# Kernel optimization log

Hardware: AMD Instinct MI355X
Metric: run time of the kernel (lower is better)

## Reference

```python
import jax, jax.numpy as jnp
import numpy as np

NUM_HEADS = 16

def setup_inputs() -> dict:
    key = jax.random.key(0)
    k1, k2, k3 = jax.random.split(key, 3)
    B, N, C = 4, 4096, 1024
    x = jax.random.normal(k1, (B, N, C), dtype=jnp.float32)
    y = jax.random.normal(k2, (B, N, C), dtype=jnp.float32)
    # nn.Linear(embed_dim, embed_dim): weight [C, C], bias [C]
    W_proj = jax.random.normal(k3, (C, C), dtype=jnp.float32) * (1.0 / np.sqrt(C))
    b_proj = jnp.zeros((C,), dtype=jnp.float32)
    return {"x": x, "y": y, "W_proj": W_proj, "b_proj": b_proj}

def reference(x, y, W_proj, b_proj):
    B, N, C = x.shape
    H = NUM_HEADS
    d = C // H
    # NOTE: no head transpose in the original -> scores are over the HEAD axis.
    q = x.reshape(B, N, H, d)
    k = y.reshape(B, N, H, d)
    v = y.reshape(B, N, H, d)
    # attn: [B, N, H, H], per-token head-to-head scores
    attn = jnp.einsum('bnhd,bngd->bnhg', q, k) / jnp.sqrt(jnp.asarray(d, x.dtype))
    attn = jax.nn.softmax(attn, axis=-1)
    # dropout(p=0.1) is identity in eval mode
    o = jnp.einsum('bnhg,bngd->bnhd', attn, v)          # [B, N, H, d]
    # x.transpose(1, 2).reshape(B, N, C) in torch:
    o = jnp.transpose(o, (0, 2, 1, 3)).reshape(B, N, C)
    out = o @ W_proj.T + b_proj
    return out
```

## Files before the change

### kernel.cpp

```cpp
#include <hip/hip_runtime.h>
#include <hip/hip_bf16.h>
#include <stdint.h>

typedef __attribute__((ext_vector_type(8))) short bf16x8;
typedef __attribute__((ext_vector_type(4))) short bf16x4;
typedef __attribute__((ext_vector_type(4))) float f32x4;
typedef __attribute__((ext_vector_type(4))) int   i32x4;

static __device__ __forceinline__ short f2bs(float f) {
  __hip_bfloat16 h = __float2bfloat16(f);
  return __builtin_bit_cast(short, h);
}

__device__ __forceinline__ void gload_lds16(const void* g, void* l) {
  auto* gp = reinterpret_cast<__attribute__((address_space(1))) uint32_t*>((uintptr_t)g);
  auto* lp = reinterpret_cast<__attribute__((address_space(3))) uint32_t*>((uintptr_t)l);
  __builtin_amdgcn_global_load_lds(gp, lp, 16, 0, 0);
}

__global__ __launch_bounds__(256) void attn_kernel(
    const float* __restrict__ x, const float* __restrict__ y,
    __hip_bfloat16* __restrict__ A)
{
  const int wid  = threadIdx.x >> 6;
  const int lane = threadIdx.x & 63;
  const int tok  = blockIdx.x * 4 + wid;
  const int b    = tok >> 12;
  const int n    = tok & 4095;

  const float* xr = x + (size_t)tok * 1024;
  const float* yr = y + (size_t)tok * 1024;

  const int c  = lane & 15;
  const int qq = lane >> 4;

  const int fbase = c * 64 + qq * 8;
  bf16x8 yf[2], xf[2];
  #pragma unroll
  for (int kk = 0; kk < 2; ++kk) {
    const float4 a0 = *(const float4*)(yr + fbase + kk * 32);
    const float4 a1 = *(const float4*)(yr + fbase + kk * 32 + 4);
    const float4 b0 = *(const float4*)(xr + fbase + kk * 32);
    const float4 b1 = *(const float4*)(xr + fbase + kk * 32 + 4);
    yf[kk] = bf16x8{f2bs(a0.x), f2bs(a0.y), f2bs(a0.z), f2bs(a0.w),
                    f2bs(a1.x), f2bs(a1.y), f2bs(a1.z), f2bs(a1.w)};
    xf[kk] = bf16x8{f2bs(b0.x), f2bs(b0.y), f2bs(b0.z), f2bs(b0.w),
                    f2bs(b1.x), f2bs(b1.y), f2bs(b1.z), f2bs(b1.w)};
  }

  f32x4 acc = {0.f, 0.f, 0.f, 0.f};
  acc = __builtin_amdgcn_mfma_f32_16x16x32_bf16(yf[0], xf[0], acc, 0, 0, 0);
  acc = __builtin_amdgcn_mfma_f32_16x16x32_bf16(yf[1], xf[1], acc, 0, 0, 0);

  float sc[4];
  #pragma unroll
  for (int r = 0; r < 4; ++r) sc[r] = acc[r] * 0.125f;
  float mx = fmaxf(fmaxf(sc[0], sc[1]), fmaxf(sc[2], sc[3]));
  mx = fmaxf(mx, __shfl_xor(mx, 16));
  mx = fmaxf(mx, __shfl_xor(mx, 32));
  float e[4];
  #pragma unroll
  for (int r = 0; r < 4; ++r) e[r] = __expf(sc[r] - mx);
  float sm = (e[0] + e[1]) + (e[2] + e[3]);
  sm += __shfl_xor(sm, 16);
  sm += __shfl_xor(sm, 32);
  const float inv = 1.0f / sm;
  float p[4];
  #pragma unroll
  for (int r = 0; r < 4; ++r) p[r] = e[r] * inv;

  f32x4 o[4];
  #pragma unroll
  for (int q = 0; q < 4; ++q) o[q] = f32x4{0.f, 0.f, 0.f, 0.f};

#if __has_builtin(__builtin_amdgcn_mfma_f32_16x16x16bf16_1k)
  const bf16x4 pa = {f2bs(p[0]), f2bs(p[1]), f2bs(p[2]), f2bs(p[3])};
  #pragma unroll
  for (int q = 0; q < 4; ++q) {
    bf16x4 bq;
    #pragma unroll
    for (int j = 0; j < 4; ++j)
      bq[j] = f2bs(yr[(qq * 4 + j) * 64 + q * 16 + c]);
    o[q] = __builtin_amdgcn_mfma_f32_16x16x16bf16_1k(pa, bq, o[q], 0, 0, 0);
  }
#else
  const int u0 = ((int)(unsigned short)f2bs(p[1]) << 16) | (unsigned short)f2bs(p[0]);
  const int u1 = ((int)(unsigned short)f2bs(p[3]) << 16) | (unsigned short)f2bs(p[2]);
  const int s0 = c + 32 * qq;
  int a0 = __shfl(u0, s0), a1 = __shfl(u1, s0);
  int a2 = __shfl(u0, s0 + 16), a3 = __shfl(u1, s0 + 16);
  const bool valid = (qq < 2);
  if (!valid) { a0 = 0; a1 = 0; a2 = 0; a3 = 0; }
  const bf16x8 a8 = __builtin_bit_cast(bf16x8, i32x4{a0, a1, a2, a3});
  #pragma unroll
  for (int q = 0; q < 4; ++q) {
    bf16x8 b8;
    #pragma unroll
    for (int j = 0; j < 8; ++j) {
      const int g = (qq * 8 + j) & 15;
      const float v = yr[g * 64 + q * 16 + c];
      b8[j] = valid ? f2bs(v) : (short)0;
    }
    o[q] = __builtin_amdgcn_mfma_f32_16x16x32_bf16(a8, b8, o[q], 0, 0, 0);
  }
#endif

  const size_t base = ((size_t)b * 4096 + (n >> 4)) * 1024 + ((n & 15) << 6) + c;
  #pragma unroll
  for (int q = 0; q < 4; ++q)
    #pragma unroll
    for (int r = 0; r < 4; ++r) {
      const int h = qq * 4 + r;
      A[base + (size_t)h * 262144 + q * 16] = __float2bfloat16(o[q][r]);
    }
}

__global__ __launch_bounds__(256) void wcvt_kernel(const float* __restrict__ w,
                                                   __hip_bfloat16* __restrict__ wb)
{
  const int i = (blockIdx.x * 256 + threadIdx.x) * 4;
  const float4 v = *(const float4*)(w + i);
  wb[i + 0] = __float2bfloat16(v.x);
  wb[i + 1] = __float2bfloat16(v.y);
  wb[i + 2] = __float2bfloat16(v.z);
  wb[i + 3] = __float2bfloat16(v.w);
}

#define NT 16

#define FENCE asm volatile("" ::: "memory")
#define BAR   __builtin_amdgcn_s_barrier()

#define STAGE_A(toff, b) do {                                           \
    gload_lds16(aSrc + (toff),          aDst + (b) * 32768);            \
    gload_lds16(aSrc + (toff) + 131072, aDst + (b) * 32768 + 8192);     \
    gload_lds16(aSrc + (toff) + 262144, aDst + (b) * 32768 + 16384);    \
    gload_lds16(aSrc + (toff) + 393216, aDst + (b) * 32768 + 24576);    \
  } while (0)

#define STAGE_B(toff, b) do {                                           \
    gload_lds16(bSrc + (toff),          bDst + (b) * 32768);            \
    gload_lds16(bSrc + (toff) + 131072, bDst + (b) * 32768 + 8192);     \
    gload_lds16(bSrc + (toff) + 262144, bDst + (b) * 32768 + 16384);    \
    gload_lds16(bSrc + (toff) + 393216, bDst + (b) * 32768 + 24576);    \
  } while (0)

__global__ __launch_bounds__(512, 2) void gemm256(
    const __hip_bfloat16* __restrict__ A,
    const __hip_bfloat16* __restrict__ Bw,
    const float* __restrict__ bias,
    float* __restrict__ C)
{
  constexpr int K = 1024, Nn = 1024;
  __shared__ char ldsA[2 * 32768];
  __shared__ char ldsB[2 * 32768];

  const int tid  = threadIdx.x;
  const int lane = tid & 63;
  const int wid  = tid >> 6;
  const int wr   = wid >> 2;
  const int wc   = wid & 3;

  const int bid = blockIdx.x;
  const int nb  = (bid & 7) * 32 + (bid >> 3);
  const int mBase = (nb >> 2) * 256;
  const int nBase = (nb & 3) * 256;

  const int srow = tid >> 3;
  const int pcb  = (tid & 7) << 4;
  const int lcb  = pcb ^ ((srow & 7) << 4);
  const char* aSrc = (const char*)A  + ((size_t)(mBase + srow) * K) * 2 + lcb;
  const char* bSrc = (const char*)Bw + ((size_t)(nBase + srow) * K) * 2 + lcb;
  char* aDst = ldsA + tid * 16;
  char* bDst = ldsB + tid * 16;

  const int fr = lane & 15;
  const int kq = lane >> 4;
  const int xr = (fr & 7) << 4;
  const int ofk0 = ((kq << 4))      ^ xr;
  const int ofk1 = (64 + (kq << 4)) ^ xr;
  const char* aRow = ldsA + (wr * 128 + fr) * 128;
  const char* bRow = ldsB + (wc * 64  + fr) * 128;

  f32x4 acc[8][4];
  #pragma unroll
  for (int m = 0; m < 8; ++m)
    #pragma unroll
    for (int n = 0; n < 4; ++n) acc[m][n] = f32x4{0.f, 0.f, 0.f, 0.f};

  STAGE_A(0, 0);
  STAGE_B(0, 0);
  asm volatile("s_waitcnt vmcnt(0)" ::: "memory");
  BAR;

  for (int t = 0; t < NT; ++t) {
    const int cur  = t & 1;
    const int nxt  = cur ^ 1;
    const int toff = (t + 1) * 128;
    const char* aR = aRow + cur * 32768;
    const char* bR = bRow + cur * 32768;
    bf16x8 Af[4], Bf[4];

    if (t + 1 < NT) STAGE_A(toff, nxt);
    #pragma unroll
    for (int n = 0; n < 4; ++n) Bf[n] = *(const bf16x8*)(bR + n * 2048 + ofk0);
    #pragma unroll
    for (int m = 0; m < 4; ++m) Af[m] = *(const bf16x8*)(aR + m * 2048 + ofk0);
    FENCE; BAR;
    asm volatile("s_waitcnt lgkmcnt(0)" ::: "memory");
    __builtin_amdgcn_sched_barrier(0);
    __builtin_amdgcn_s_setprio(1);
    #pragma unroll
    for (int m = 0; m < 4; ++m)
      #pragma unroll
      for (int n = 0; n < 4; ++n)
        acc[m][n] = __builtin_amdgcn_mfma_f32_16x16x32_bf16(Af[m], Bf[n], acc[m][n], 0, 0, 0);
    __builtin_amdgcn_s_setprio(0);
    FENCE; BAR;

    if (t + 1 < NT) STAGE_B(toff, nxt);
    #pragma unroll
    for (int m = 0; m < 4; ++m) Af[m] = *(const bf16x8*)(aR + (4 + m) * 2048 + ofk0);
    FENCE; BAR;
    asm volatile("s_waitcnt lgkmcnt(0)" ::: "memory");
    __builtin_amdgcn_sched_barrier(0);
    __builtin_amdgcn_s_setprio(1);
    #pragma unroll
    for (int m = 0; m < 4; ++m)
      #pragma unroll
      for (int n = 0; n < 4; ++n)
        acc[4 + m][n] = __builtin_amdgcn_mfma_f32_16x16x32_bf16(Af[m], Bf[n], acc[4 + m][n], 0, 0, 0);
    __builtin_amdgcn_s_setprio(0);
    FENCE; BAR;

    #pragma unroll
    for (int n = 0; n < 4; ++n) Bf[n] = *(const bf16x8*)(bR + n * 2048 + ofk1);
    #pragma unroll
    for (int m = 0; m < 4; ++m) Af[m] = *(const bf16x8*)(aR + m * 2048 + ofk1);
    FENCE; BAR;
    asm volatile("s_waitcnt lgkmcnt(0)" ::: "memory");
    __builtin_amdgcn_sched_barrier(0);
    __builtin_amdgcn_s_setprio(1);
    #pragma unroll
    for (int m = 0; m < 4; ++m)
      #pragma unroll
      for (int n = 0; n < 4; ++n)
        acc[m][n] = __builtin_amdgcn_mfma_f32_16x16x32_bf16(Af[m], Bf[n], acc[m][n], 0, 0, 0);
    __builtin_amdgcn_s_setprio(0);
    FENCE; BAR;

    #pragma unroll
    for (int m = 0; m < 4; ++m) Af[m] = *(const bf16x8*)(aR + (4 + m) * 2048 + ofk1);
    FENCE; BAR;
    asm volatile("s_waitcnt lgkmcnt(0)" ::: "memory");
    __builtin_amdgcn_sched_barrier(0);
    __builtin_amdgcn_s_setprio(1);
    #pragma unroll
    for (int m = 0; m < 4; ++m)
      #pragma unroll
      for (int n = 0; n < 4; ++n)
        acc[4 + m][n] = __builtin_amdgcn_mfma_f32_16x16x32_bf16(Af[m], Bf[n], acc[4 + m][n], 0, 0, 0);
    __builtin_amdgcn_s_setprio(0);
    if (t + 1 < NT) asm volatile("s_waitcnt vmcnt(0)" ::: "memory");
    FENCE; BAR;
  }

  const int fq = lane >> 4;
  #pragma unroll
  for (int n = 0; n < 4; ++n) {
    const int col = nBase + wc * 64 + n * 16 + fr;
    const float bv = bias[col];
    #pragma unroll
    for (int m = 0; m < 8; ++m) {
      const int row0 = mBase + wr * 128 + m * 16 + fq * 4;
      #pragma unroll
      for (int r = 0; r < 4; ++r)
        C[(size_t)(row0 + r) * Nn + col] = acc[m][n][r] + bv;
    }
  }
}

extern "C" void kernel_launch(void* const* d_in, const int* in_sizes, int n_in,
                              void* d_out, int out_size, void* d_ws, size_t ws_size,
                              hipStream_t stream) {
  const float* x    = (const float*)d_in[0];
  const float* y    = (const float*)d_in[1];
  const float* W    = (const float*)d_in[2];
  const float* bias = (const float*)d_in[3];
  float* out = (float*)d_out;

  __hip_bfloat16* Abuf = (__hip_bfloat16*)d_ws;
  __hip_bfloat16* Wbuf = (__hip_bfloat16*)((char*)d_ws + (size_t)16384 * 1024 * 2);

  wcvt_kernel<<<1024, 256, 0, stream>>>(W, Wbuf);
  attn_kernel<<<4096, 256, 0, stream>>>(x, y, Abuf);
  gemm256<<<256, 512, 0, stream>>>(Abuf, Wbuf, bias, out);
}
```

Before: 76.39 us.

## Split GEMM tile prefetch into finer chunks with partial vmcnt waits and peeled epilogue

Global-to-LDS staging of the next A/B K-tile is split into pairs of loads spread across the four MFMA phases. Full vmcnt(0) drains are replaced with vmcnt(2) partial waits so only the chunks needed next must arrive. The last iteration is peeled so the stores for the first half of the accumulators overlap the final MFMA phase. This aims to hide load latency and epilogue store cost, at the risk of tighter ordering assumptions around the partial waits and LDS buffer reuse.

```diff
diff --git a/kernel.cpp b/kernel.cpp
--- a/kernel.cpp
+++ b/kernel.cpp
@@ -130,20 +130,30 @@
 
 #define FENCE asm volatile("" ::: "memory")
 #define BAR   __builtin_amdgcn_s_barrier()
-
-#define STAGE_A(toff, b) do {                                           \
-    gload_lds16(aSrc + (toff),          aDst + (b) * 32768);            \
-    gload_lds16(aSrc + (toff) + 131072, aDst + (b) * 32768 + 8192);     \
-    gload_lds16(aSrc + (toff) + 262144, aDst + (b) * 32768 + 16384);    \
-    gload_lds16(aSrc + (toff) + 393216, aDst + (b) * 32768 + 24576);    \
-  } while (0)
-
-#define STAGE_B(toff, b) do {                                           \
-    gload_lds16(bSrc + (toff),          bDst + (b) * 32768);            \
-    gload_lds16(bSrc + (toff) + 131072, bDst + (b) * 32768 + 8192);     \
-    gload_lds16(bSrc + (toff) + 262144, bDst + (b) * 32768 + 16384);    \
-    gload_lds16(bSrc + (toff) + 393216, bDst + (b) * 32768 + 24576);    \
-  } while (0)
+#define LGKM0 asm volatile("s_waitcnt lgkmcnt(0)" ::: "memory")
+#define VM2   asm volatile("s_waitcnt vmcnt(2)" ::: "memory")
+#define VM0   asm volatile("s_waitcnt vmcnt(0)" ::: "memory")
+#define SB0   __builtin_amdgcn_sched_barrier(0)
+#define SP1   __builtin_amdgcn_s_setprio(1)
+#define SP0   __builtin_amdgcn_s_setprio(0)
+
+#define SGA(j, toff, bufn) gload_lds16(aSrc + (toff) + (j) * 131072, aDst + (bufn) * 32768 + (j) * 8192)
+#define SGB(j, toff, bufn) gload_lds16(bSrc + (toff) + (j) * 131072, bDst + (bufn) * 32768 + (j) * 8192)
+
+#define MFMA16(MO)                                                         \
+  _Pragma("unroll")                                                        \
+  for (int m = 0; m < 4; ++m)                                              \
+    _Pragma("unroll")                                                      \
+    for (int n = 0; n < 4; ++n)                                            \
+      acc[(MO) + m][n] = __builtin_amdgcn_mfma_f32_16x16x32_bf16(Af[m], Bf[n], acc[(MO) + m][n], 0, 0, 0)
+
+#define READ_B(OF)                                                         \
+  _Pragma("unroll")                                                        \
+  for (int n = 0; n < 4; ++n) Bf[n] = *(const bf16x8*)(bR + n * 2048 + (OF))
+
+#define READ_A(MO, OF)                                                     \
+  _Pragma("unroll")                                                        \
+  for (int m = 0; m < 4; ++m) Af[m] = *(const bf16x8*)(aR + ((MO) + m) * 2048 + (OF))
 
 __global__ __launch_bounds__(512, 2) void gemm256(
     const __hip_bfloat16* __restrict__ A,
@@ -167,8 +177,7 @@
   const int nBase = (nb & 3) * 256;
 
   const int srow = tid >> 3;
-  const int pcb  = (tid & 7) << 4;
-  const int lcb  = pcb ^ ((srow & 7) << 4);
+  const int lcb  = ((tid & 7) << 4) ^ ((srow & 7) << 4);
   const char* aSrc = (const char*)A  + ((size_t)(mBase + srow) * K) * 2 + lcb;
   const char* bSrc = (const char*)Bw + ((size_t)(nBase + srow) * K) * 2 + lcb;
   char* aDst = ldsA + tid * 16;
@@ -188,12 +197,12 @@
     #pragma unroll
     for (int n = 0; n < 4; ++n) acc[m][n] = f32x4{0.f, 0.f, 0.f, 0.f};
 
-  STAGE_A(0, 0);
-  STAGE_B(0, 0);
-  asm volatile("s_waitcnt vmcnt(0)" ::: "memory");
+  SGB(0, 0, 0); SGB(1, 0, 0); SGB(2, 0, 0); SGB(3, 0, 0);
+  SGA(0, 0, 0); SGA(2, 0, 0); SGA(1, 0, 0); SGA(3, 0, 0);
+  VM2;
   BAR;
 
-  for (int t = 0; t < NT; ++t) {
+  for (int t = 0; t < NT - 1; ++t) {
     const int cur  = t & 1;
     const int nxt  = cur ^ 1;
     const int toff = (t + 1) * 128;
@@ -201,77 +210,72 @@
     const char* bR = bRow + cur * 32768;
     bf16x8 Af[4], Bf[4];
 
-    if (t + 1 < NT) STAGE_A(toff, nxt);
-    #pragma unroll
-    for (int n = 0; n < 4; ++n) Bf[n] = *(const bf16x8*)(bR + n * 2048 + ofk0);
-    #pragma unroll
-    for (int m = 0; m < 4; ++m) Af[m] = *(const bf16x8*)(aR + m * 2048 + ofk0);
+    SGB(0, toff, nxt); SGB(1, toff, nxt);
+    READ_B(ofk0); READ_A(0, ofk0);
+    FENCE; BAR; LGKM0; SB0;
+    SP1; MFMA16(0); SP0;
+    VM2; FENCE; BAR;
+
+    SGB(2, toff, nxt); SGB(3, toff, nxt);
+    READ_A(4, ofk0);
+    FENCE; BAR; LGKM0; SB0;
+    SP1; MFMA16(4); SP0;
     FENCE; BAR;
-    asm volatile("s_waitcnt lgkmcnt(0)" ::: "memory");
-    __builtin_amdgcn_sched_barrier(0);
-    __builtin_amdgcn_s_setprio(1);
-    #pragma unroll
-    for (int m = 0; m < 4; ++m)
+
+    SGA(0, toff, nxt); SGA(2, toff, nxt);
+    READ_B(ofk1); READ_A(0, ofk1);
+    FENCE; BAR; LGKM0; SB0;
+    SP1; MFMA16(0); SP0;
+    FENCE; BAR;
+
+    SGA(1, toff, nxt); SGA(3, toff, nxt);
+    READ_A(4, ofk1);
+    FENCE; BAR; LGKM0; SB0;
+    SP1; MFMA16(4); SP0;
+    VM2; FENCE; BAR;
+  }
+
+  const int fq = lane >> 4;
+  {
+    const char* aR = aRow + ((NT - 1) & 1) * 32768;
+    const char* bR = bRow + ((NT - 1) & 1) * 32768;
+    bf16x8 Af[4], Bf[4];
+
+    READ_B(ofk0); READ_A(0, ofk0);
+    FENCE; BAR; LGKM0; SB0;
+    SP1; MFMA16(0); SP0;
+    VM0; FENCE; BAR;
+    READ_A(4, ofk0);
+    FENCE; BAR; LGKM0; SB0;
+    SP1; MFMA16(4); SP0;
+    FENCE; BAR;
+    READ_B(ofk1); READ_A(0, ofk1);
+    FENCE; BAR; LGKM0; SB0;
+    SP1; MFMA16(0); SP0;
+    #pragma unroll
+    for (int n = 0; n < 4; ++n) {
+      const int col = nBase + wc * 64 + n * 16 + fr;
+      const float bv = bias[col];
       #pragma unroll
-      for (int n = 0; n < 4; ++n)
-        acc[m][n] = __builtin_amdgcn_mfma_f32_16x16x32_bf16(Af[m], Bf[n], acc[m][n], 0, 0, 0);
-    __builtin_amdgcn_s_setprio(0);
+      for (int m = 0; m < 4; ++m) {
+        const int row0 = mBase + wr * 128 + m * 16 + fq * 4;
+        #pragma unroll
+        for (int r = 0; r < 4; ++r)
+          C[(size_t)(row0 + r) * Nn + col] = acc[m][n][r] + bv;
+      }
+    }
     FENCE; BAR;
-
-    if (t + 1 < NT) STAGE_B(toff, nxt);
-    #pragma unroll
-    for (int m = 0; m < 4; ++m) Af[m] = *(const bf16x8*)(aR + (4 + m) * 2048 + ofk0);
-    FENCE; BAR;
-    asm volatile("s_waitcnt lgkmcnt(0)" ::: "memory");
-    __builtin_amdgcn_sched_barrier(0);
-    __builtin_amdgcn_s_setprio(1);
-    #pragma unroll
-    for (int m = 0; m < 4; ++m)
-      #pragma unroll
-      for (int n = 0; n < 4; ++n)
-        acc[4 + m][n] = __builtin_amdgcn_mfma_f32_16x16x32_bf16(Af[m], Bf[n], acc[4 + m][n], 0, 0, 0);
-    __builtin_amdgcn_s_setprio(0);
-    FENCE; BAR;
-
-    #pragma unroll
-    for (int n = 0; n < 4; ++n) Bf[n] = *(const bf16x8*)(bR + n * 2048 + ofk1);
-    #pragma unroll
-    for (int m = 0; m < 4; ++m) Af[m] = *(const bf16x8*)(aR + m * 2048 + ofk1);
-    FENCE; BAR;
-    asm volatile("s_waitcnt lgkmcnt(0)" ::: "memory");
-    __builtin_amdgcn_sched_barrier(0);
-    __builtin_amdgcn_s_setprio(1);
-    #pragma unroll
-    for (int m = 0; m < 4; ++m)
-      #pragma unroll
-      for (int n = 0; n < 4; ++n)
-        acc[m][n] = __builtin_amdgcn_mfma_f32_16x16x32_bf16(Af[m], Bf[n], acc[m][n], 0, 0, 0);
-    __builtin_amdgcn_s_setprio(0);
-    FENCE; BAR;
-
-    #pragma unroll
-    for (int m = 0; m < 4; ++m) Af[m] = *(const bf16x8*)(aR + (4 + m) * 2048 + ofk1);
-    FENCE; BAR;
-    asm volatile("s_waitcnt lgkmcnt(0)" ::: "memory");
-    __builtin_amdgcn_sched_barrier(0);
-    __builtin_amdgcn_s_setprio(1);
-    #pragma unroll
-    for (int m = 0; m < 4; ++m)
-      #pragma unroll
-      for (int n = 0; n < 4; ++n)
-        acc[4 + m][n] = __builtin_amdgcn_mfma_f32_16x16x32_bf16(Af[m], Bf[n], acc[4 + m][n], 0, 0, 0);
-    __builtin_amdgcn_s_setprio(0);
-    if (t + 1 < NT) asm volatile("s_waitcnt vmcnt(0)" ::: "memory");
-    FENCE; BAR;
-  }
-
-  const int fq = lane >> 4;
+    READ_A(4, ofk1);
+    FENCE; BAR; LGKM0; SB0;
+    SP1; MFMA16(4); SP0;
+  }
+
   #pragma unroll
   for (int n = 0; n < 4; ++n) {
     const int col = nBase + wc * 64 + n * 16 + fr;
     const float bv = bias[col];
     #pragma unroll
-    for (int m = 0; m < 8; ++m) {
+    for (int m = 4; m < 8; ++m) {
       const int row0 = mBase + wr * 128 + m * 16 + fq * 4;
       #pragma unroll
       for (int r = 0; r < 4; ++r)
```

After: 75.27 us. No clear change (-1.5%).
